# Performance work log

Hardware: AMD Instinct MI355X
Metric: run time of the kernel (lower is better)

Reference implementation:

```python
import jax, jax.numpy as jnp
import numpy as np

DEGREE = 4
NUM_CHARTS = 8
N = 16384
IN_DIM = 29  # 3*(2*4+1) + 2 procedural params


def positional_encoding(x, degree=DEGREE):
    # Faithful to torch order: [x, sin(2^1 pi x), cos(2^1 pi x), ..., sin(2^d pi x), cos(2^d pi x)]
    pe = [x]
    for d in range(1, degree + 1):
        s = (2.0 ** d) * np.pi
        pe.append(jnp.sin(s * x))
        pe.append(jnp.cos(s * x))
    return jnp.concatenate(pe, axis=-1)


def setup_inputs() -> dict:
    key = jax.random.key(0)
    ks = jax.random.split(key, 9)
    h = 256
    sc = 0.05
    return {
        "x": jax.random.normal(ks[0], (N, 3), jnp.float32),
        "proc": jax.random.normal(ks[1], (1, 2), jnp.float32),
        "W0": jax.random.normal(ks[2], (NUM_CHARTS, IN_DIM, h), jnp.float32) * sc,
        "b0": jax.random.normal(ks[3], (NUM_CHARTS, h), jnp.float32) * sc,
        "Wh": jax.random.normal(ks[4], (NUM_CHARTS, 6, h, h), jnp.float32) * sc,
        "bh": jax.random.normal(ks[5], (NUM_CHARTS, 6, h), jnp.float32) * sc,
        "Wl": jax.random.normal(ks[6], (NUM_CHARTS, h, 2), jnp.float32) * sc,
        "bl": jax.random.normal(ks[7], (NUM_CHARTS, 2), jnp.float32) * sc,
        "mlp_idx": jax.random.randint(ks[8], (N,), 0, NUM_CHARTS, jnp.int32),
    }


def reference(x, proc, W0, b0, Wh, bh, Wl, bl, mlp_idx):
    xp = positional_encoding(x)                      # (N, 27)
    proc_rep = jnp.broadcast_to(proc, (xp.shape[0], proc.shape[1]))
    xp = jnp.concatenate([xp, proc_rep], axis=-1)    # (N, 29)

    out = jnp.zeros((xp.shape[0], Wl.shape[-1]), xp.dtype)
    n_hidden = Wh.shape[1]
    for c in range(NUM_CHARTS):                      # small fixed chart loop
        h = jax.nn.relu(xp @ W0[c] + b0[c])          # (N, 256)
        for l in range(n_hidden):
            h = jax.nn.relu(h @ Wh[c, l] + bh[c, l])
        oc = jax.nn.sigmoid(h @ Wl[c] + bl[c])       # (N, 2)
        out = jnp.where((mlp_idx == c)[:, None], oc, out)
    return out
```

## Files before the change

kernel.cpp:

```cpp
#include <hip/hip_runtime.h>
#include <hip/hip_bf16.h>
#include <math.h>

#define NPTS   16384
#define NCH    8
#define MT     64
#define LSTR   272
#define SEG    16384

typedef short bf16x8 __attribute__((ext_vector_type(8)));
typedef float f32x4  __attribute__((ext_vector_type(4)));

__device__ __forceinline__ float bf2f(unsigned short u){
  union { unsigned int i; float f; } v; v.i = ((unsigned int)u) << 16; return v.f;
}
__device__ __forceinline__ unsigned short f2bf(float f){
  union { float f; unsigned int i; } v; v.f = f;
  unsigned int x = v.i;
  return (unsigned short)((x + 0x7fffu + ((x >> 16) & 1u)) >> 16);
}


__global__ __launch_bounds__(256) void prep_k(
    const float* __restrict__ Wh, const float* __restrict__ W0,
    const int* __restrict__ midx,
    unsigned short* __restrict__ Wth, unsigned short* __restrict__ Wt0,
    int* __restrict__ cursors, int* __restrict__ bucket){
  int bid = blockIdx.x, tid = threadIdx.x;
  if (bid < 768){
    __shared__ __align__(16) float tile[64][68];
    int mat = bid >> 4;
    int t4  = bid & 15;
    int kr  = (t4 >> 2) << 6;
    int nc  = (t4 & 3) << 6;
    const float* src = Wh + (size_t)mat * 65536;
    unsigned short* dst = Wth + (size_t)mat * 65536;
    int r  = tid >> 2;
    int cs = (tid & 3) << 4;
    const float* sp = &src[(kr + r) * 256 + nc + cs];
    *(float4*)&tile[r][cs]      = *(const float4*)&sp[0];
    *(float4*)&tile[r][cs + 4]  = *(const float4*)&sp[4];
    *(float4*)&tile[r][cs + 8]  = *(const float4*)&sp[8];
    *(float4*)&tile[r][cs + 12] = *(const float4*)&sp[12];
    __syncthreads();
    int n  = tid >> 2;
    int ks = (tid & 3) << 4;
    __align__(16) unsigned short tmp[16];
    #pragma unroll
    for (int j = 0; j < 16; j++) tmp[j] = f2bf(tile[ks + j][n]);
    *(uint4*)&dst[(nc + n) * 256 + kr + ks]     = *(const uint4*)&tmp[0];
    *(uint4*)&dst[(nc + n) * 256 + kr + ks + 8] = *(const uint4*)&tmp[8];
  } else if (bid < 776){
    int c = bid - 768;
    for (int j = 0; j < 32; j++){
      int i = j * 256 + tid;
      int k = i & 31, n = i >> 5;
      unsigned short v = 0;
      if (k < 29) v = f2bf(W0[(c * 29 + k) * 256 + n]);
      Wt0[c * 8192 + i] = v;
    }
  } else {
    __shared__ int wcnt[4][NCH];
    __shared__ int woff[4][NCH];
    int i = (bid - 776) * 256 + tid;
    int c = midx[i];
    int lane = tid & 63, wv4 = tid >> 6;
    int rk = 0;
    #pragma unroll
    for (int cc = 0; cc < NCH; cc++){
      unsigned long long m = __ballot(c == cc);
      if (lane == cc) wcnt[wv4][cc] = __popcll(m);
      if (c == cc) rk = __popcll(m & ((1ull << lane) - 1));
    }
    __syncthreads();
    if (tid < NCH){
      int c8 = tid;
      int t0 = wcnt[0][c8], t1 = wcnt[1][c8], t2 = wcnt[2][c8], t3 = wcnt[3][c8];
      int gb = atomicAdd(&cursors[c8], t0 + t1 + t2 + t3);
      woff[0][c8] = gb; woff[1][c8] = gb + t0;
      woff[2][c8] = gb + t0 + t1; woff[3][c8] = gb + t0 + t1 + t2;
    }
    __syncthreads();
    bucket[c * SEG + woff[wv4][c] + rk] = i;
  }
}


__global__ __launch_bounds__(256, 1) void mlp_k(
    const float* __restrict__ x,
    const float* __restrict__ proc,
    const float* __restrict__ b0,
    const float* __restrict__ bh,
    const float* __restrict__ Wl,
    const float* __restrict__ bl,
    const unsigned short* __restrict__ Wt0,
    const unsigned short* __restrict__ Wth,
    const int* __restrict__ counts,
    const int* __restrict__ bucket,
    float* __restrict__ out)
{
  __shared__ __align__(16) unsigned short act0[MT * LSTR];
  __shared__ __align__(16) unsigned short act1[MT * LSTR];
  __shared__ float biasb[7 * 256];
  __shared__ float wlb[512];
  __shared__ int ridx[MT];

  int chart = blockIdx.x & 7;
  int tile  = blockIdx.x >> 3;
  int cnt   = counts[chart] - tile * MT;
  if (cnt <= 0) return;
  if (cnt > MT) cnt = MT;

  int tid  = threadIdx.x;
  int lane = tid & 63;
  int wv   = tid >> 6;
  int l15  = lane & 15;
  int quad = lane >> 4;
  int nb   = wv * 64;

  biasb[tid] = b0[chart * 256 + tid];
  #pragma unroll
  for (int j = 0; j < 6; j++)
    biasb[(j + 1) * 256 + tid] = bh[(chart * 6 + j) * 256 + tid];
  wlb[tid]       = Wl[chart * 512 + tid];
  wlb[256 + tid] = Wl[chart * 512 + 256 + tid];

  if (tid < MT){
    int row = tid;
    int g = (row < cnt) ? bucket[chart * SEG + tile * MT + row] : -1;
    ridx[row] = g;
    unsigned short* rowp = &act0[row * LSTR];
    if (g >= 0){
      float xv0 = x[g*3+0], xv1 = x[g*3+1], xv2 = x[g*3+2];
      rowp[0] = f2bf(xv0); rowp[1] = f2bf(xv1); rowp[2] = f2bf(xv2);
      #pragma unroll
      for (int d = 1; d <= 4; d++){
        float s = (float)(1 << d) * 3.14159265358979323846f;
        int o = 3 + (d - 1) * 6;
        rowp[o+0] = f2bf(sinf(s*xv0)); rowp[o+1] = f2bf(sinf(s*xv1)); rowp[o+2] = f2bf(sinf(s*xv2));
        rowp[o+3] = f2bf(cosf(s*xv0)); rowp[o+4] = f2bf(cosf(s*xv1)); rowp[o+5] = f2bf(cosf(s*xv2));
      }
      rowp[27] = f2bf(proc[0]); rowp[28] = f2bf(proc[1]);
      rowp[29] = 0; rowp[30] = 0; rowp[31] = 0;
    } else {
      #pragma unroll
      for (int k = 0; k < 32; k++) rowp[k] = 0;
    }
  }
  __syncthreads();

  f32x4 acc[4][4];
  const f32x4 zz = {0.f, 0.f, 0.f, 0.f};

  {
    const unsigned short* W0p = Wt0 + chart * 8192;
    bf16x8 b0r[4];
    #pragma unroll
    for (int nt = 0; nt < 4; nt++)
      b0r[nt] = *(const bf16x8*)&W0p[(nb + nt * 16 + l15) * 32 + quad * 8];
    #pragma unroll
    for (int mt = 0; mt < 4; mt++){
      bf16x8 a0 = *(const bf16x8*)&act0[(mt * 16 + l15) * LSTR + quad * 8];
      #pragma unroll
      for (int nt = 0; nt < 4; nt++)
        acc[mt][nt] = __builtin_amdgcn_mfma_f32_16x16x32_bf16(a0, b0r[nt], zz, 0, 0, 0);
    }
    #pragma unroll
    for (int nt = 0; nt < 4; nt++){
      int col = nb + nt * 16 + l15;
      float bias = biasb[col];
      #pragma unroll
      for (int mt = 0; mt < 4; mt++)
        #pragma unroll
        for (int r = 0; r < 4; r++){
          float v = acc[mt][nt][r] + bias;
          v = v > 0.f ? v : 0.f;
          act1[(mt * 16 + quad * 4 + r) * LSTR + col] = f2bf(v);
        }
    }
  }
  __syncthreads();

  for (int l = 1; l <= 6; l++){
    const unsigned short* wp = Wth + ((size_t)(chart * 6 + l - 1) << 16)
                             + (size_t)(nb + l15) * 256 + quad * 8;
    const unsigned short* ain = (l & 1) ? act1 : act0;
    unsigned short* aout      = (l & 1) ? act0 : act1;

    bf16x8 breg[8][4];
    #pragma unroll
    for (int kk = 0; kk < 8; kk++)
      #pragma unroll
      for (int nt = 0; nt < 4; nt++)
        breg[kk][nt] = *(const bf16x8*)&wp[nt * 4096 + kk * 32];

    #pragma unroll
    for (int mt = 0; mt < 4; mt++){
      bf16x8 a[8];
      #pragma unroll
      for (int kk = 0; kk < 8; kk++)
        a[kk] = *(const bf16x8*)&ain[(mt * 16 + l15) * LSTR + kk * 32 + quad * 8];
      #pragma unroll
      for (int kk = 0; kk < 8; kk++)
        #pragma unroll
        for (int nt = 0; nt < 4; nt++)
          acc[mt][nt] = __builtin_amdgcn_mfma_f32_16x16x32_bf16(
              a[kk], breg[kk][nt], (kk == 0) ? zz : acc[mt][nt], 0, 0, 0);
    }

    #pragma unroll
    for (int nt = 0; nt < 4; nt++){
      int col = nb + nt * 16 + l15;
      float bias = biasb[l * 256 + col];
      #pragma unroll
      for (int mt = 0; mt < 4; mt++)
        #pragma unroll
        for (int r = 0; r < 4; r++){
          float v = acc[mt][nt][r] + bias;
          v = v > 0.f ? v : 0.f;
          aout[(mt * 16 + quad * 4 + r) * LSTR + col] = f2bf(v);
        }
    }
    __syncthreads();
  }

  {
    int m = tid >> 2;
    int p = tid & 3;
    const unsigned short* hrow = act1 + m * LSTR + p * 64;
    const float* wlp = wlb + p * 128;
    float s0 = 0.f, s1 = 0.f;
    #pragma unroll 8
    for (int k = 0; k < 64; k += 2){
      float4 w4 = *(const float4*)&wlp[k * 2];
      unsigned int h2 = *(const unsigned int*)&hrow[k];
      float hv0 = bf2f((unsigned short)(h2 & 0xffff));
      float hv1 = bf2f((unsigned short)(h2 >> 16));
      s0 += hv0 * w4.x + hv1 * w4.z;
      s1 += hv0 * w4.y + hv1 * w4.w;
    }
    s0 += __shfl_xor(s0, 1); s0 += __shfl_xor(s0, 2);
    s1 += __shfl_xor(s1, 1); s1 += __shfl_xor(s1, 2);
    if (p == 0){
      int g = ridx[m];
      if (g >= 0){
        float o0 = 1.f / (1.f + __expf(-(s0 + bl[chart*2+0])));
        float o1 = 1.f / (1.f + __expf(-(s1 + bl[chart*2+1])));
        *(float2*)&out[(size_t)g * 2] = make_float2(o0, o1);
      }
    }
  }
}


extern "C" void kernel_launch(void* const* d_in, const int* in_sizes, int n_in,
                              void* d_out, int out_size, void* d_ws, size_t ws_size,
                              hipStream_t stream){
  const float* x    = (const float*)d_in[0];
  const float* proc = (const float*)d_in[1];
  const float* W0   = (const float*)d_in[2];
  const float* b0   = (const float*)d_in[3];
  const float* Wh   = (const float*)d_in[4];
  const float* bh   = (const float*)d_in[5];
  const float* Wl   = (const float*)d_in[6];
  const float* bl   = (const float*)d_in[7];
  const int* midx = (const int*)d_in[8];
  float* out = (float*)d_out;

  char* ws = (char*)d_ws;
  int* cursors = (int*)ws;
  int* bucket  = cursors + 8;
  size_t off = (((size_t)(8 + NCH * SEG)) * 4 + 15) & ~(size_t)15;
  unsigned short* Wt0 = (unsigned short*)(ws + off);
  unsigned short* Wth = Wt0 + NCH * 8192;

  hipMemsetAsync(cursors, 0, 8 * sizeof(int), stream);
  hipLaunchKernelGGL(prep_k, dim3(840),  dim3(256), 0, stream,
                     Wh, W0, midx, Wth, Wt0, cursors, bucket);
  hipLaunchKernelGGL(mlp_k,  dim3(2048), dim3(256), 0, stream,
                     x, proc, b0, bh, Wl, bl, Wt0, Wth, cursors, bucket, out);
}
```

Measured before the change: 144.2 us.

## Stream hidden-layer weights into LDS with double-buffered async DMA chunks

Result: slower. 181.1 us (+25.6%).

```diff
diff --git a/kernel.cpp b/kernel.cpp
--- a/kernel.cpp
+++ b/kernel.cpp
@@ -5,8 +5,9 @@
 #define NPTS   16384
 #define NCH    8
 #define MT     64
-#define LSTR   272
+#define LSTR   264
 #define SEG    16384
+#define CPAD   64
 
 typedef short bf16x8 __attribute__((ext_vector_type(8)));
 typedef float f32x4  __attribute__((ext_vector_type(4)));
@@ -18,6 +19,11 @@
   union { float f; unsigned int i; } v; v.f = f;
   unsigned int x = v.i;
   return (unsigned short)((x + 0x7fffu + ((x >> 16) & 1u)) >> 16);
+}
+__device__ __forceinline__ void dma16(const void* g, void* l){
+  __builtin_amdgcn_global_load_lds(
+      (const __attribute__((address_space(1))) unsigned int*)g,
+      (__attribute__((address_space(3))) unsigned int*)l, 16, 0, 0);
 }
 
 
@@ -27,66 +33,87 @@
     unsigned short* __restrict__ Wth, unsigned short* __restrict__ Wt0,
     int* __restrict__ cursors, int* __restrict__ bucket){
   int bid = blockIdx.x, tid = threadIdx.x;
-  if (bid < 768){
-    __shared__ __align__(16) float tile[64][68];
-    int mat = bid >> 4;
-    int t4  = bid & 15;
-    int kr  = (t4 >> 2) << 6;
-    int nc  = (t4 & 3) << 6;
-    const float* src = Wh + (size_t)mat * 65536;
-    unsigned short* dst = Wth + (size_t)mat * 65536;
-    int r  = tid >> 2;
-    int cs = (tid & 3) << 4;
-    const float* sp = &src[(kr + r) * 256 + nc + cs];
-    *(float4*)&tile[r][cs]      = *(const float4*)&sp[0];
-    *(float4*)&tile[r][cs + 4]  = *(const float4*)&sp[4];
-    *(float4*)&tile[r][cs + 8]  = *(const float4*)&sp[8];
-    *(float4*)&tile[r][cs + 12] = *(const float4*)&sp[12];
-    __syncthreads();
-    int n  = tid >> 2;
-    int ks = (tid & 3) << 4;
-    __align__(16) unsigned short tmp[16];
-    #pragma unroll
-    for (int j = 0; j < 16; j++) tmp[j] = f2bf(tile[ks + j][n]);
-    *(uint4*)&dst[(nc + n) * 256 + kr + ks]     = *(const uint4*)&tmp[0];
-    *(uint4*)&dst[(nc + n) * 256 + kr + ks + 8] = *(const uint4*)&tmp[8];
-  } else if (bid < 776){
-    int c = bid - 768;
-    for (int j = 0; j < 32; j++){
-      int i = j * 256 + tid;
-      int k = i & 31, n = i >> 5;
-      unsigned short v = 0;
-      if (k < 29) v = f2bf(W0[(c * 29 + k) * 256 + n]);
-      Wt0[c * 8192 + i] = v;
+  if (bid < 192){
+    __shared__ __align__(16) unsigned short tile[64 * LSTR];
+    int mat = bid >> 2, ck = bid & 3;
+    const float* src = Wh + (size_t)mat * 65536 + (size_t)ck * 64 * 256;
+    int r = tid >> 2, seg = (tid & 3) * 64;
+    const float* sp = &src[r * 256 + seg];
+    #pragma unroll
+    for (int j8 = 0; j8 < 8; j8++){
+      float4 f0 = *(const float4*)&sp[j8 * 8];
+      float4 f1 = *(const float4*)&sp[j8 * 8 + 4];
+      __align__(16) unsigned short t8[8];
+      t8[0]=f2bf(f0.x); t8[1]=f2bf(f0.y); t8[2]=f2bf(f0.z); t8[3]=f2bf(f0.w);
+      t8[4]=f2bf(f1.x); t8[5]=f2bf(f1.y); t8[6]=f2bf(f1.z); t8[7]=f2bf(f1.w);
+      *(uint4*)&tile[r * LSTR + seg + j8 * 8] = *(const uint4*)t8;
+    }
+    __syncthreads();
+    unsigned short* dst = Wth + (size_t)mat * 65536 + (size_t)ck * 16384;
+    #pragma unroll
+    for (int it = 0; it < 8; it++){
+      int s = it * 256 + tid;
+      int k8l = s >> 8, n = s & 255;
+      __align__(16) unsigned short t8[8];
+      #pragma unroll
+      for (int j = 0; j < 8; j++) t8[j] = tile[(k8l * 8 + j) * LSTR + n];
+      *(uint4*)&dst[(size_t)s * 8] = *(const uint4*)t8;
+    }
+  } else if (bid < 200){
+    int c = bid - 192;
+    #pragma unroll
+    for (int it = 0; it < 4; it++){
+      int s = it * 256 + tid;
+      int k8 = s >> 8, n = s & 255;
+      __align__(16) unsigned short t8[8];
+      #pragma unroll
+      for (int j = 0; j < 8; j++){
+        int k = k8 * 8 + j;
+        t8[j] = (k < 29) ? f2bf(W0[(c * 29 + k) * 256 + n]) : (unsigned short)0;
+      }
+      *(uint4*)&Wt0[(size_t)c * 8192 + (size_t)s * 8] = *(const uint4*)t8;
     }
   } else {
-    __shared__ int wcnt[4][NCH];
-    __shared__ int woff[4][NCH];
-    int i = (bid - 776) * 256 + tid;
-    int c = midx[i];
-    int lane = tid & 63, wv4 = tid >> 6;
-    int rk = 0;
-    #pragma unroll
-    for (int cc = 0; cc < NCH; cc++){
-      unsigned long long m = __ballot(c == cc);
-      if (lane == cc) wcnt[wv4][cc] = __popcll(m);
-      if (c == cc) rk = __popcll(m & ((1ull << lane) - 1));
-    }
-    __syncthreads();
-    if (tid < NCH){
-      int c8 = tid;
-      int t0 = wcnt[0][c8], t1 = wcnt[1][c8], t2 = wcnt[2][c8], t3 = wcnt[3][c8];
-      int gb = atomicAdd(&cursors[c8], t0 + t1 + t2 + t3);
-      woff[0][c8] = gb; woff[1][c8] = gb + t0;
-      woff[2][c8] = gb + t0 + t1; woff[3][c8] = gb + t0 + t1 + t2;
-    }
-    __syncthreads();
-    bucket[c * SEG + woff[wv4][c] + rk] = i;
-  }
-}
-
-
-__global__ __launch_bounds__(256, 1) void mlp_k(
+    __shared__ int h[NCH], cur[NCH];
+    int seg = bid - 200;
+    int lane = tid & 63;
+    if (tid < NCH) h[tid] = 0;
+    __syncthreads();
+    for (int it = 0; it < 8; it++){
+      int i = seg * 2048 + it * 256 + tid;
+      int c = midx[i];
+      #pragma unroll
+      for (int cc = 0; cc < NCH; cc++){
+        unsigned long long m = __ballot(c == cc);
+        if (m && lane == (int)(__ffsll((long long)m) - 1))
+          atomicAdd(&h[cc], (int)__popcll(m));
+      }
+    }
+    __syncthreads();
+    if (tid < NCH) cur[tid] = atomicAdd(&cursors[tid * CPAD], h[tid]);
+    __syncthreads();
+    for (int it = 0; it < 8; it++){
+      int i = seg * 2048 + it * 256 + tid;
+      int c = midx[i];
+      #pragma unroll
+      for (int cc = 0; cc < NCH; cc++){
+        unsigned long long m = __ballot(c == cc);
+        if (!m) continue;
+        int leader = (int)(__ffsll((long long)m) - 1);
+        int wb = 0;
+        if (lane == leader) wb = atomicAdd(&cur[cc], (int)__popcll(m));
+        wb = __shfl(wb, leader);
+        if (c == cc){
+          int rk = (int)__popcll(m & ((1ull << lane) - 1));
+          bucket[cc * SEG + wb + rk] = i;
+        }
+      }
+    }
+  }
+}
+
+
+__global__ __launch_bounds__(256) void mlp_k(
     const float* __restrict__ x,
     const float* __restrict__ proc,
     const float* __restrict__ b0,
@@ -99,15 +126,16 @@
     const int* __restrict__ bucket,
     float* __restrict__ out)
 {
-  __shared__ __align__(16) unsigned short act0[MT * LSTR];
-  __shared__ __align__(16) unsigned short act1[MT * LSTR];
+  __shared__ __align__(16) unsigned short actA[MT * LSTR];
+  __shared__ __align__(16) unsigned short actB[MT * LSTR];
+  __shared__ __align__(16) unsigned short wbuf[2][16384];
   __shared__ float biasb[7 * 256];
   __shared__ float wlb[512];
   __shared__ int ridx[MT];
 
   int chart = blockIdx.x & 7;
   int tile  = blockIdx.x >> 3;
-  int cnt   = counts[chart] - tile * MT;
+  int cnt   = counts[chart * CPAD] - tile * MT;
   if (cnt <= 0) return;
   if (cnt > MT) cnt = MT;
 
@@ -116,7 +144,29 @@
   int wv   = tid >> 6;
   int l15  = lane & 15;
   int quad = lane >> 4;
-  int nb   = wv * 64;
+  int cb   = wv * 64;
+
+  const unsigned short* Wc = Wth + ((size_t)(chart * 6) << 16);
+
+  #define ISSUE(l, ck, buf) do {                                              \
+    const unsigned short* src_ = Wc + (((size_t)((l) - 1)) << 16)             \
+                               + (((size_t)(ck)) << 14);                      \
+    _Pragma("unroll")                                                         \
+    for (int it = 0; it < 8; it++){                                           \
+      int sb = (wv * 8 + it) * 64;                                            \
+      dma16(src_ + (size_t)(sb + lane) * 8, &wbuf[buf][(size_t)sb * 8]);      \
+    }                                                                         \
+  } while (0)
+
+  {
+    const unsigned short* s0 = Wt0 + chart * 8192;
+    #pragma unroll
+    for (int it = 0; it < 4; it++){
+      int sb = (wv * 4 + it) * 64;
+      dma16(s0 + (size_t)(sb + lane) * 8, &wbuf[0][(size_t)sb * 8]);
+    }
+  }
+  ISSUE(1, 0, 1);
 
   biasb[tid] = b0[chart * 256 + tid];
   #pragma unroll
@@ -129,7 +179,7 @@
     int row = tid;
     int g = (row < cnt) ? bucket[chart * SEG + tile * MT + row] : -1;
     ridx[row] = g;
-    unsigned short* rowp = &act0[row * LSTR];
+    unsigned short* rowp = &actA[row * LSTR];
     if (g >= 0){
       float xv0 = x[g*3+0], xv1 = x[g*3+1], xv2 = x[g*3+2];
       rowp[0] = f2bf(xv0); rowp[1] = f2bf(xv1); rowp[2] = f2bf(xv2);
@@ -153,21 +203,21 @@
   const f32x4 zz = {0.f, 0.f, 0.f, 0.f};
 
   {
-    const unsigned short* W0p = Wt0 + chart * 8192;
-    bf16x8 b0r[4];
-    #pragma unroll
-    for (int nt = 0; nt < 4; nt++)
-      b0r[nt] = *(const bf16x8*)&W0p[(nb + nt * 16 + l15) * 32 + quad * 8];
-    #pragma unroll
-    for (int mt = 0; mt < 4; mt++){
-      bf16x8 a0 = *(const bf16x8*)&act0[(mt * 16 + l15) * LSTR + quad * 8];
-      #pragma unroll
-      for (int nt = 0; nt < 4; nt++)
-        acc[mt][nt] = __builtin_amdgcn_mfma_f32_16x16x32_bf16(a0, b0r[nt], zz, 0, 0, 0);
-    }
+    bf16x8 a0[4];
+    #pragma unroll
+    for (int mt = 0; mt < 4; mt++)
+      a0[mt] = *(const bf16x8*)&actA[(mt * 16 + l15) * LSTR + quad * 8];
     #pragma unroll
     for (int nt = 0; nt < 4; nt++){
-      int col = nb + nt * 16 + l15;
+      int slot = quad * 256 + cb + nt * 16 + l15;
+      bf16x8 b = *(const bf16x8*)&wbuf[0][slot * 8];
+      #pragma unroll
+      for (int mt = 0; mt < 4; mt++)
+        acc[mt][nt] = __builtin_amdgcn_mfma_f32_16x16x32_bf16(a0[mt], b, zz, 0, 0, 0);
+    }
+    #pragma unroll
+    for (int nt = 0; nt < 4; nt++){
+      int col = cb + nt * 16 + l15;
       float bias = biasb[col];
       #pragma unroll
       for (int mt = 0; mt < 4; mt++)
@@ -175,59 +225,63 @@
         for (int r = 0; r < 4; r++){
           float v = acc[mt][nt][r] + bias;
           v = v > 0.f ? v : 0.f;
-          act1[(mt * 16 + quad * 4 + r) * LSTR + col] = f2bf(v);
+          actB[(mt * 16 + quad * 4 + r) * LSTR + col] = f2bf(v);
         }
     }
   }
+
+  for (int lc = 0; lc < 24; lc++){
+    int l = 1 + (lc >> 2), ck = lc & 3, buf = (lc + 1) & 1;
+    __syncthreads();
+    if (lc + 1 < 24){
+      int lc2 = lc + 1;
+      ISSUE(1 + (lc2 >> 2), lc2 & 3, lc & 1);
+    }
+    const unsigned short* ain = (l & 1) ? actB : actA;
+    unsigned short* aout      = (l & 1) ? actA : actB;
+
+    bf16x8 a[4][2];
+    #pragma unroll
+    for (int mt = 0; mt < 4; mt++)
+      #pragma unroll
+      for (int kl = 0; kl < 2; kl++)
+        a[mt][kl] = *(const bf16x8*)&ain[(mt * 16 + l15) * LSTR + ck * 64 + kl * 32 + quad * 8];
+
+    #pragma unroll
+    for (int kl = 0; kl < 2; kl++)
+      #pragma unroll
+      for (int nt = 0; nt < 4; nt++){
+        int slot = (kl * 4 + quad) * 256 + cb + nt * 16 + l15;
+        bf16x8 b = *(const bf16x8*)&wbuf[buf][slot * 8];
+        #pragma unroll
+        for (int mt = 0; mt < 4; mt++){
+          f32x4 cin = (ck == 0 && kl == 0) ? zz : acc[mt][nt];
+          acc[mt][nt] = __builtin_amdgcn_mfma_f32_16x16x32_bf16(a[mt][kl], b, cin, 0, 0, 0);
+        }
+      }
+
+    if (ck == 3){
+      #pragma unroll
+      for (int nt = 0; nt < 4; nt++){
+        int col = cb + nt * 16 + l15;
+        float bias = biasb[l * 256 + col];
+        #pragma unroll
+        for (int mt = 0; mt < 4; mt++)
+          #pragma unroll
+          for (int r = 0; r < 4; r++){
+            float v = acc[mt][nt][r] + bias;
+            v = v > 0.f ? v : 0.f;
+            aout[(mt * 16 + quad * 4 + r) * LSTR + col] = f2bf(v);
+          }
+      }
+    }
+  }
   __syncthreads();
-
-  for (int l = 1; l <= 6; l++){
-    const unsigned short* wp = Wth + ((size_t)(chart * 6 + l - 1) << 16)
-                             + (size_t)(nb + l15) * 256 + quad * 8;
-    const unsigned short* ain = (l & 1) ? act1 : act0;
-    unsigned short* aout      = (l & 1) ? act0 : act1;
-
-    bf16x8 breg[8][4];
-    #pragma unroll
-    for (int kk = 0; kk < 8; kk++)
-      #pragma unroll
-      for (int nt = 0; nt < 4; nt++)
-        breg[kk][nt] = *(const bf16x8*)&wp[nt * 4096 + kk * 32];
-
-    #pragma unroll
-    for (int mt = 0; mt < 4; mt++){
-      bf16x8 a[8];
-      #pragma unroll
-      for (int kk = 0; kk < 8; kk++)
-        a[kk] = *(const bf16x8*)&ain[(mt * 16 + l15) * LSTR + kk * 32 + quad * 8];
-      #pragma unroll
-      for (int kk = 0; kk < 8; kk++)
-        #pragma unroll
-        for (int nt = 0; nt < 4; nt++)
-          acc[mt][nt] = __builtin_amdgcn_mfma_f32_16x16x32_bf16(
-              a[kk], breg[kk][nt], (kk == 0) ? zz : acc[mt][nt], 0, 0, 0);
-    }
-
-    #pragma unroll
-    for (int nt = 0; nt < 4; nt++){
-      int col = nb + nt * 16 + l15;
-      float bias = biasb[l * 256 + col];
-      #pragma unroll
-      for (int mt = 0; mt < 4; mt++)
-        #pragma unroll
-        for (int r = 0; r < 4; r++){
-          float v = acc[mt][nt][r] + bias;
-          v = v > 0.f ? v : 0.f;
-          aout[(mt * 16 + quad * 4 + r) * LSTR + col] = f2bf(v);
-        }
-    }
-    __syncthreads();
-  }
 
   {
     int m = tid >> 2;
     int p = tid & 3;
-    const unsigned short* hrow = act1 + m * LSTR + p * 64;
+    const unsigned short* hrow = actB + m * LSTR + p * 64;
     const float* wlp = wlb + p * 128;
     float s0 = 0.f, s1 = 0.f;
     #pragma unroll 8
@@ -269,13 +323,13 @@
 
   char* ws = (char*)d_ws;
   int* cursors = (int*)ws;
-  int* bucket  = cursors + 8;
-  size_t off = (((size_t)(8 + NCH * SEG)) * 4 + 15) & ~(size_t)15;
+  int* bucket  = cursors + NCH * CPAD;
+  size_t off = (((size_t)(NCH * CPAD + NCH * SEG)) * 4 + 15) & ~(size_t)15;
   unsigned short* Wt0 = (unsigned short*)(ws + off);
   unsigned short* Wth = Wt0 + NCH * 8192;
 
-  hipMemsetAsync(cursors, 0, 8 * sizeof(int), stream);
-  hipLaunchKernelGGL(prep_k, dim3(840),  dim3(256), 0, stream,
+  hipMemsetAsync(cursors, 0, NCH * CPAD * sizeof(int), stream);
+  hipLaunchKernelGGL(prep_k, dim3(208),  dim3(256), 0, stream,
                      Wh, W0, midx, Wth, Wt0, cursors, bucket);
   hipLaunchKernelGGL(mlp_k,  dim3(2048), dim3(256), 0, stream,
                      x, proc, b0, bh, Wl, bl, Wt0, Wth, cursors, bucket, out);
```
